# Kernel optimization log

Hardware: AMD Instinct MI355X
Metric: run time of the kernel (lower is better)

## Reference

```python
import jax, jax.numpy as jnp
import numpy as np

N_SAMPLE = 32
RADIUS = 0.25
NORMALIZE_DP = True

B, N, K, C = 8, 8192, 2048, 64


def setup_inputs() -> dict:
    key = jax.random.key(0)
    k1, k2, k3 = jax.random.split(key, 3)
    points = jax.random.uniform(k1, (B, N, 3), dtype=jnp.float32)
    centroids = jax.random.uniform(k2, (B, K, 3), dtype=jnp.float32)
    features = jax.random.normal(k3, (B, C, N), dtype=jnp.float32)
    return {"points": points, "centroids": centroids, "features": features}


def _ball_query(points, centroids, n_sample, radius):
    # points: (B,N,3), centroids: (B,K,3) -> indices (B,K,n_sample) int32
    # squared distances via |c|^2 + |p|^2 - 2 c.p to avoid a (B,K,N,3) temp
    cp = jnp.einsum("bkd,bnd->bkn", centroids, points)  # (B,K,N)
    d2 = (
        jnp.sum(centroids * centroids, -1)[:, :, None]
        + jnp.sum(points * points, -1)[:, None, :]
        - 2.0 * cp
    )
    mask = d2 < radius * radius  # (B,K,N)
    # stable argsort on ~mask puts in-ball indices first, in ascending order
    order = jnp.argsort(jnp.logical_not(mask), axis=-1, stable=True)
    idx = order[..., :n_sample]  # (B,K,S)
    count = jnp.sum(mask, axis=-1, keepdims=True)  # (B,K,1)
    slot = jnp.arange(n_sample)[None, None, :]
    # CUDA ball_query semantics: pad empty slots with the first found index
    idx = jnp.where(slot < count, idx, idx[..., :1])
    return idx


def reference(points, centroids, features):
    idx = _ball_query(points, centroids, N_SAMPLE, RADIUS)  # (B,K,S)
    # gather points: (B,K,S,3)
    gp = jax.vmap(lambda p, i: p[i])(points, idx)
    gp = gp - centroids[:, :, None, :]  # centroid subtract
    if NORMALIZE_DP:
        gp = gp / RADIUS
    grouped_pts = jnp.transpose(gp, (0, 3, 1, 2))  # (B,3,K,S)
    # gather features: (B,C,K,S)
    new_feats = jax.vmap(lambda f, i: f[:, i])(features, idx)
    return grouped_pts, new_feats
```

## Files before the change

### kernel.cpp

```cpp
#include <hip/hip_runtime.h>

constexpr int B = 8;
constexpr int N = 8192;
constexpr int K = 2048;
constexpr int C = 64;
constexpr int NS = 32;
#define RAD2 0.0625f

typedef float  fx4 __attribute__((ext_vector_type(4)));
typedef int    ix4 __attribute__((ext_vector_type(4)));

__global__ __launch_bounds__(128) void ballquery_gp_kernel(
    const float* __restrict__ points,
    const float* __restrict__ centroids,
    float* __restrict__ gp_out,
    int* __restrict__ idx_ws)
{
#pragma clang fp contract(off)
    __shared__ unsigned long long masks_s[2][N / 64];
    const int wave = (blockIdx.x * blockDim.x + threadIdx.x) >> 6;
    const int lane = threadIdx.x & 63;
    if (wave >= B * K) return;
    const int b = wave >> 11;
    const int k = wave & (K - 1);
    unsigned long long* mk = masks_s[threadIdx.x >> 6];

    const float* cptr = centroids + (size_t)(b * K + k) * 3;
    const float c0 = cptr[0], c1 = cptr[1], c2 = cptr[2];
    const float cc = (c0 * c0 + c1 * c1) + c2 * c2;

    const float* pbase = points + (size_t)b * N * 3;

    int count = 0;

    float a0 = pbase[lane * 3 + 0];
    float a1 = pbase[lane * 3 + 1];
    float a2 = pbase[lane * 3 + 2];
    float e0 = pbase[(lane + 64) * 3 + 0];
    float e1 = pbase[(lane + 64) * 3 + 1];
    float e2 = pbase[(lane + 64) * 3 + 2];

    int g = 0;
    for (int base = 0; base < N; base += 128) {
        const bool more = (base + 128 < N);
        const int nlo = more ? (base + 128 + lane) : lane;
        const int nhi = more ? (base + 192 + lane) : lane;
        const float na0 = pbase[nlo * 3 + 0];
        const float na1 = pbase[nlo * 3 + 1];
        const float na2 = pbase[nlo * 3 + 2];
        const float ne0 = pbase[nhi * 3 + 0];
        const float ne1 = pbase[nhi * 3 + 1];
        const float ne2 = pbase[nhi * 3 + 2];

        const float ppA = (a0 * a0 + a1 * a1) + a2 * a2;
        const float cpA = (c0 * a0 + c1 * a1) + c2 * a2;
        const float d2A = (cc + ppA) - 2.0f * cpA;
        const float ppE = (e0 * e0 + e1 * e1) + e2 * e2;
        const float cpE = (c0 * e0 + c1 * e1) + c2 * e2;
        const float d2E = (cc + ppE) - 2.0f * cpE;

        const unsigned long long mlo = __ballot(d2A < RAD2);
        const unsigned long long mhi = __ballot(d2E < RAD2);
        if (lane == 0) {
            mk[g] = mlo;
            mk[g + 1] = mhi;
        }
        count += __popcll(mlo) + __popcll(mhi);
        g += 2;
        if (count >= NS) break;
        a0 = na0; a1 = na1; a2 = na2;
        e0 = ne0; e1 = ne1; e2 = ne2;
    }

    if (lane < NS) {
        const int cnt = count < NS ? count : NS;
        int i = 0;
        if (count > 0) {
            const int target = (lane < cnt) ? lane : 0;
            int running = 0;
            int gg = 0;
            unsigned long long m;
            for (;; ++gg) {
                m = mk[gg];
                const int c = __popcll(m);
                if (running + c > target) break;
                running += c;
            }
            int r = target - running;
            for (int t = 0; t < r; ++t) m &= m - 1;
            i = gg * 64 + __builtin_ctzll(m);
        }
        const float p0 = pbase[i * 3 + 0];
        const float p1 = pbase[i * 3 + 1];
        const float p2 = pbase[i * 3 + 2];
        idx_ws[(size_t)wave * NS + lane] = i;
        float* gpb = gp_out + ((size_t)b * 3 * K + k) * NS;
        gpb[0 * K * NS + lane] = (p0 - c0) * 4.0f;
        gpb[1 * K * NS + lane] = (p1 - c1) * 4.0f;
        gpb[2 * K * NS + lane] = (p2 - c2) * 4.0f;
    }
}

__global__ __launch_bounds__(1024) void gather_feats_lds(
    const float* __restrict__ features,
    const int* __restrict__ idx_ws,
    float* __restrict__ nf_out)
{
    __shared__ float row[N];
    const int bc = blockIdx.x;
    const int t = threadIdx.x;

    {
        const fx4* frow4 = reinterpret_cast<const fx4*>(features + (size_t)bc * N);
        fx4* row4 = reinterpret_cast<fx4*>(row);
#pragma unroll
        for (int j = 0; j < 2; ++j)
            row4[t + j * 1024] = __builtin_nontemporal_load(&frow4[t + j * 1024]);
    }
    __syncthreads();

    const int b = bc >> 6;
    const int* idxb = idx_ws + (size_t)b * K * NS;
    float* outb = nf_out + (size_t)bc * K * NS;

    ix4 iv = *reinterpret_cast<const ix4*>(idxb + (size_t)t * 4);
#pragma unroll
    for (int j = 0; j < 16; ++j) {
        const int g = j * 1024 + t;
        ix4 ivn;
        if (j < 15)
            ivn = *reinterpret_cast<const ix4*>(idxb + (size_t)(g + 1024) * 4);
        fx4 v;
        v.x = row[iv.x];
        v.y = row[iv.y];
        v.z = row[iv.z];
        v.w = row[iv.w];
        __builtin_nontemporal_store(v, reinterpret_cast<fx4*>(outb + (size_t)g * 4));
        if (j < 15) iv = ivn;
    }
}

extern "C" void kernel_launch(void* const* d_in, const int* in_sizes, int n_in,
                              void* d_out, int out_size, void* d_ws, size_t ws_size,
                              hipStream_t stream) {
    const float* points    = (const float*)d_in[0];
    const float* centroids = (const float*)d_in[1];
    const float* features  = (const float*)d_in[2];
    float* out = (float*)d_out;

    float* gp_out = out;
    float* nf_out = out + (size_t)B * 3 * K * NS;
    int* idx_ws = (int*)d_ws;

    const int waves = B * K;

    hipLaunchKernelGGL(ballquery_gp_kernel, dim3(waves / 2), dim3(128), 0, stream,
                       points, centroids, gp_out, idx_ws);

    hipLaunchKernelGGL(gather_feats_lds, dim3(B * C), dim3(1024), 0, stream,
                       features, idx_ws, nf_out);
}
```

Measured before the change: 51.82 us.

## Pack points into float4 with precomputed norm and batch the ball-query scan

Adds a pre-pass that repacks points into float4 (x,y,z,|p|^2) in workspace, so the ball query can use single 16-byte vector loads and skip recomputing point norms for every centroid. The first 1024 points are loaded eagerly into 16 registers, which raises memory-level parallelism for the usual early exit. Later points are scanned 256 at a time. The cost is an extra kernel launch, an extra workspace write/read, and higher register pressure that may lower occupancy.

Measured after the change: 58.77 us. 13.4% more time.

```diff
diff --git a/kernel.cpp b/kernel.cpp
--- a/kernel.cpp
+++ b/kernel.cpp
@@ -9,67 +9,82 @@
 
 typedef float  fx4 __attribute__((ext_vector_type(4)));
 typedef int    ix4 __attribute__((ext_vector_type(4)));
+typedef unsigned long long ull;
+
+__global__ __launch_bounds__(256) void pack_points_kernel(
+    const float* __restrict__ points,
+    fx4* __restrict__ pts4)
+{
+#pragma clang fp contract(off)
+    const int i = blockIdx.x * blockDim.x + threadIdx.x;
+    const float p0 = points[(size_t)i * 3 + 0];
+    const float p1 = points[(size_t)i * 3 + 1];
+    const float p2 = points[(size_t)i * 3 + 2];
+    fx4 v;
+    v.x = p0; v.y = p1; v.z = p2;
+    v.w = (p0 * p0 + p1 * p1) + p2 * p2;
+    pts4[i] = v;
+}
 
 __global__ __launch_bounds__(128) void ballquery_gp_kernel(
-    const float* __restrict__ points,
+    const fx4* __restrict__ pts4,
     const float* __restrict__ centroids,
     float* __restrict__ gp_out,
     int* __restrict__ idx_ws)
 {
 #pragma clang fp contract(off)
-    __shared__ unsigned long long masks_s[2][N / 64];
+    __shared__ ull masks_s[2][N / 64];
     const int wave = (blockIdx.x * blockDim.x + threadIdx.x) >> 6;
     const int lane = threadIdx.x & 63;
     if (wave >= B * K) return;
     const int b = wave >> 11;
     const int k = wave & (K - 1);
-    unsigned long long* mk = masks_s[threadIdx.x >> 6];
+    ull* mk = masks_s[threadIdx.x >> 6];
 
     const float* cptr = centroids + (size_t)(b * K + k) * 3;
     const float c0 = cptr[0], c1 = cptr[1], c2 = cptr[2];
     const float cc = (c0 * c0 + c1 * c1) + c2 * c2;
 
-    const float* pbase = points + (size_t)b * N * 3;
+    const fx4* p4 = pts4 + (size_t)b * N;
 
     int count = 0;
 
-    float a0 = pbase[lane * 3 + 0];
-    float a1 = pbase[lane * 3 + 1];
-    float a2 = pbase[lane * 3 + 2];
-    float e0 = pbase[(lane + 64) * 3 + 0];
-    float e1 = pbase[(lane + 64) * 3 + 1];
-    float e2 = pbase[(lane + 64) * 3 + 2];
+    fx4 buf[16];
+#pragma unroll
+    for (int gg = 0; gg < 16; ++gg)
+        buf[gg] = p4[gg * 64 + lane];
+#pragma unroll
+    for (int gg = 0; gg < 16; ++gg) {
+        const float cp = (c0 * buf[gg].x + c1 * buf[gg].y) + c2 * buf[gg].z;
+        const float d2 = (cc + buf[gg].w) - 2.0f * cp;
+        const ull m = __ballot(d2 < RAD2);
+        if (lane == 0) mk[gg] = m;
+        count += __popcll(m);
+    }
 
-    int g = 0;
-    for (int base = 0; base < N; base += 128) {
-        const bool more = (base + 128 < N);
-        const int nlo = more ? (base + 128 + lane) : lane;
-        const int nhi = more ? (base + 192 + lane) : lane;
-        const float na0 = pbase[nlo * 3 + 0];
-        const float na1 = pbase[nlo * 3 + 1];
-        const float na2 = pbase[nlo * 3 + 2];
-        const float ne0 = pbase[nhi * 3 + 0];
-        const float ne1 = pbase[nhi * 3 + 1];
-        const float ne2 = pbase[nhi * 3 + 2];
+    if (count < NS) {
+        int g = 16;
+        for (int base = 1024; base < N; base += 256) {
+            const fx4 s0 = p4[base + lane];
+            const fx4 s1 = p4[base + 64 + lane];
+            const fx4 s2 = p4[base + 128 + lane];
+            const fx4 s3 = p4[base + 192 + lane];
 
-        const float ppA = (a0 * a0 + a1 * a1) + a2 * a2;
-        const float cpA = (c0 * a0 + c1 * a1) + c2 * a2;
-        const float d2A = (cc + ppA) - 2.0f * cpA;
-        const float ppE = (e0 * e0 + e1 * e1) + e2 * e2;
-        const float cpE = (c0 * e0 + c1 * e1) + c2 * e2;
-        const float d2E = (cc + ppE) - 2.0f * cpE;
-
-        const unsigned long long mlo = __ballot(d2A < RAD2);
-        const unsigned long long mhi = __ballot(d2E < RAD2);
-        if (lane == 0) {
-            mk[g] = mlo;
-            mk[g + 1] = mhi;
+            const float cpa = (c0 * s0.x + c1 * s0.y) + c2 * s0.z;
+            const float cpb = (c0 * s1.x + c1 * s1.y) + c2 * s1.z;
+            const float cpc = (c0 * s2.x + c1 * s2.y) + c2 * s2.z;
+            const float cpd = (c0 * s3.x + c1 * s3.y) + c2 * s3.z;
+            const ull m0 = __ballot(((cc + s0.w) - 2.0f * cpa) < RAD2);
+            const ull m1 = __ballot(((cc + s1.w) - 2.0f * cpb) < RAD2);
+            const ull m2 = __ballot(((cc + s2.w) - 2.0f * cpc) < RAD2);
+            const ull m3 = __ballot(((cc + s3.w) - 2.0f * cpd) < RAD2);
+            if (lane == 0) {
+                mk[g] = m0; mk[g + 1] = m1; mk[g + 2] = m2; mk[g + 3] = m3;
+            }
+            count += __popcll(m0) + __popcll(m1) + __popcll(m2) + __popcll(m3);
+            g += 4;
+            if (count >= NS) break;
         }
-        count += __popcll(mlo) + __popcll(mhi);
-        g += 2;
-        if (count >= NS) break;
-        a0 = na0; a1 = na1; a2 = na2;
-        e0 = ne0; e1 = ne1; e2 = ne2;
     }
 
     if (lane < NS) {
@@ -79,7 +94,7 @@
             const int target = (lane < cnt) ? lane : 0;
             int running = 0;
             int gg = 0;
-            unsigned long long m;
+            ull m;
             for (;; ++gg) {
                 m = mk[gg];
                 const int c = __popcll(m);
@@ -90,14 +105,12 @@
             for (int t = 0; t < r; ++t) m &= m - 1;
             i = gg * 64 + __builtin_ctzll(m);
         }
-        const float p0 = pbase[i * 3 + 0];
-        const float p1 = pbase[i * 3 + 1];
-        const float p2 = pbase[i * 3 + 2];
+        const fx4 p = p4[i];
         idx_ws[(size_t)wave * NS + lane] = i;
         float* gpb = gp_out + ((size_t)b * 3 * K + k) * NS;
-        gpb[0 * K * NS + lane] = (p0 - c0) * 4.0f;
-        gpb[1 * K * NS + lane] = (p1 - c1) * 4.0f;
-        gpb[2 * K * NS + lane] = (p2 - c2) * 4.0f;
+        gpb[0 * K * NS + lane] = (p.x - c0) * 4.0f;
+        gpb[1 * K * NS + lane] = (p.y - c1) * 4.0f;
+        gpb[2 * K * NS + lane] = (p.z - c2) * 4.0f;
     }
 }
 
@@ -150,12 +163,16 @@
 
     float* gp_out = out;
     float* nf_out = out + (size_t)B * 3 * K * NS;
+
     int* idx_ws = (int*)d_ws;
+    fx4* pts4   = (fx4*)((char*)d_ws + ((size_t)4 << 20));
+
+    hipLaunchKernelGGL(pack_points_kernel, dim3(B * N / 256), dim3(256), 0, stream,
+                       points, pts4);
 
     const int waves = B * K;
-
     hipLaunchKernelGGL(ballquery_gp_kernel, dim3(waves / 2), dim3(128), 0, stream,
-                       points, centroids, gp_out, idx_ws);
+                       pts4, centroids, gp_out, idx_ws);
 
     hipLaunchKernelGGL(gather_feats_lds, dim3(B * C), dim3(1024), 0, stream,
                        features, idx_ws, nf_out);
```
